# Optimization experiments

Measured on AMD Instinct MI355X. Metric: run time of the kernel, lower is better.

Reference implementation:

```python
import jax, jax.numpy as jnp
import numpy as np

N, L, D, H = 2, 2048, 1024, 16
DK = D // H  # 64


def setup_inputs() -> dict:
    key = jax.random.key(0)
    ks = jax.random.split(key, 8)
    Xq = jax.random.normal(ks[0], (N, L, D), dtype=jnp.float32)
    Xk = jax.random.normal(ks[1], (N, L, D), dtype=jnp.float32)
    Xv = jax.random.normal(ks[2], (N, L, D), dtype=jnp.float32)
    mask_2d = jax.random.randint(ks[3], (N, L, L), 0, 2, dtype=jnp.int32)
    scale = 0.02
    Wq = jax.random.normal(ks[4], (D, D), dtype=jnp.float32) * scale
    Wk = jax.random.normal(ks[5], (D, D), dtype=jnp.float32) * scale
    Wv = jax.random.normal(ks[6], (D, D), dtype=jnp.float32) * scale
    Wo = jax.random.normal(ks[7], (D, D), dtype=jnp.float32) * scale
    return {"Xq": Xq, "Xk": Xk, "Xv": Xv, "Wq": Wq, "Wk": Wk, "Wv": Wv, "Wo": Wo, "mask_2d": mask_2d}


def reference(Xq, Xk, Xv, Wq, Wk, Wv, Wo, mask_2d):
    # Projections (bias=False). Per-head slicing in the original == reshape to [N,L,H,DK].
    Q = (Xq @ Wq).reshape(N, L, H, DK)
    K = (Xk @ Wk).reshape(N, L, H, DK)
    V = (Xv @ Wv).reshape(N, L, H, DK)
    # Scaled dot-product scores: [N, H, L, L]
    scores = jnp.einsum("blhd,bmhd->bhlm", Q, K) / jnp.sqrt(jnp.asarray(DK, scores_dtype(Q)))
    # NOTE: original uses masked_fill(mask==0, 0) BEFORE softmax (zero-fill, not -inf).
    scores = jnp.where(mask_2d[:, None, :, :] == 0, jnp.zeros((), scores.dtype), scores)
    A = jax.nn.softmax(scores, axis=-1)
    O = jnp.einsum("bhlm,bmhd->blhd", A, V).reshape(N, L, D)
    return O @ Wo


def scores_dtype(Q):
    return Q.dtype
```

## Files before the change

kernel.cpp:

```cpp
#include <hip/hip_runtime.h>
#include <hip/hip_bf16.h>

#define NB 2
#define L_SEQ 2048
#define NH 16
#define DKH 64
#define DMODEL 1024
#define MROWS (NB * L_SEQ)
#define QSCALE 0.18033688f
#define DD (DMODEL * DMODEL)

typedef __attribute__((ext_vector_type(8))) short short8;
typedef __attribute__((ext_vector_type(4))) float f32x4;

static __device__ __forceinline__ unsigned short f2bf(float f) {
    unsigned u = __float_as_uint(f);
    u += 0x7fffu + ((u >> 16) & 1u);
    return (unsigned short)(u >> 16);
}

static __device__ __forceinline__ float fexp2(float x) {
#if __has_builtin(__builtin_amdgcn_exp2f)
    return __builtin_amdgcn_exp2f(x);
#else
    return __expf(x * 0.6931471806f);
#endif
}

static __device__ __forceinline__ unsigned pk_bf16(float a, float b) {
    __hip_bfloat162 h = __float22bfloat162_rn(make_float2(a, b));
    return *reinterpret_cast<unsigned*>(&h);
}

static __device__ __forceinline__ void gll16(const void* g, void* l) {
    __builtin_amdgcn_global_load_lds(
        (const __attribute__((address_space(1))) void*)g,
        (__attribute__((address_space(3))) void*)l, 16, 0, 0);
}

__global__ __launch_bounds__(256)
void prep(const float* __restrict__ Xq, const float* __restrict__ Xk,
          const float* __restrict__ Xv, const float* __restrict__ w0,
          const float* __restrict__ w1, const float* __restrict__ w2,
          const float* __restrict__ w3, const int* __restrict__ mask,
          unsigned short* __restrict__ XB, unsigned short* __restrict__ WtB,
          unsigned long long* __restrict__ MWT)
{
    __shared__ float ts[32][33];
    const int bx = blockIdx.x;
    const int t  = threadIdx.x;

    if (bx < 12288) {
        const int z = bx >> 12;
        const float* src = (z == 0) ? Xq : (z == 1) ? Xk : Xv;
        const size_t i4 = (size_t)(bx & 4095) * 256 + t;
        float4 v = ((const float4*)src)[i4];
        ushort4 o;
        o.x = f2bf(v.x); o.y = f2bf(v.y); o.z = f2bf(v.z); o.w = f2bf(v.w);
        ((ushort4*)(XB + (size_t)z * 4194304))[i4] = o;
    } else if (bx < 16384) {
        const int idx = bx - 12288;
        const int z   = idx >> 10;
        const int rem = idx & 1023;
        const float* W = (z == 0) ? w0 : (z == 1) ? w1 : (z == 2) ? w2 : w3;
        unsigned short* Wt = WtB + (size_t)z * DD;
        const int n0 = (rem & 31) * 32;
        const int k0 = (rem >> 5) * 32;
        const int r  = t >> 3;
        const int c  = (t & 7) * 4;
        float4 v = *(const float4*)&W[(size_t)(k0 + r) * DMODEL + n0 + c];
        ts[r][c + 0] = v.x; ts[r][c + 1] = v.y;
        ts[r][c + 2] = v.z; ts[r][c + 3] = v.w;
        __syncthreads();
        ushort4 o;
        o.x = f2bf(ts[c + 0][r]); o.y = f2bf(ts[c + 1][r]);
        o.z = f2bf(ts[c + 2][r]); o.w = f2bf(ts[c + 3][r]);
        *(ushort4*)&Wt[(size_t)(n0 + r) * DMODEL + k0 + c] = o;
    } else {
        const int lane = t & 63;
        const size_t wbase = (size_t)(bx - 16384) * 4 + (t >> 6);
#pragma unroll
        for (int it = 0; it < 8; ++it) {
            const size_t wid = wbase + (size_t)it * 16384;
            const int mv = mask[wid * 64 + lane];
            const unsigned long long bits = __ballot(mv != 0);
            if (lane == 0) {
                const int b   = (int)(wid >> 16);
                const int rem = (int)(wid & 65535);
                const int row = rem >> 5;
                const int wd  = rem & 31;
                MWT[((size_t)b * 32 + wd) * L_SEQ + row] = bits;
            }
        }
    }
}

__global__ __launch_bounds__(256)
void gemm_qkv(const unsigned short* __restrict__ XB,
              const unsigned short* __restrict__ WtB,
              unsigned short* __restrict__ QKV)
{
    __shared__ __align__(16) unsigned short SMEM[16384];

    const int t    = threadIdx.x;
    const int w    = t >> 6;
    const int lane = t & 63;

    const int bid   = blockIdx.x;
    const int xcd   = bid & 7;
    const int idx   = bid >> 3;
    const int pair  = xcd * 12 + (idx >> 3);
    const int n0    = (idx & 7) * 128;
    const int m0    = (pair & 31) * 128;
    const int z     = pair >> 5;

    const unsigned short* A = XB  + (size_t)z * ((size_t)MROWS * DMODEL);
    const unsigned short* B = WtB + (size_t)z * DD;

    const int srow = lane >> 2;
    const int sc4  = (lane & 3) ^ (srow & 3);

    const unsigned short* ag[2];
    const unsigned short* bg[2];
    int lao[2], lbo[2];
#pragma unroll
    for (int g = 0; g < 2; ++g) {
        const int R = w * 32 + g * 16;
        ag[g] = A + (size_t)(m0 + R + srow) * DMODEL + sc4 * 8;
        bg[g] = B + (size_t)(n0 + R + srow) * DMODEL + sc4 * 8;
        lao[g] = R * 32;
        lbo[g] = R * 32;
    }

    const int ml = lane & 15;
    const int q  = lane >> 4;
    const int wm = (w >> 1) * 64;
    const int wn = (w & 1) * 64;

    const f32x4 z4 = {0.f, 0.f, 0.f, 0.f};
    f32x4 acc[4][4];
#pragma unroll
    for (int i = 0; i < 4; ++i)
#pragma unroll
        for (int j = 0; j < 4; ++j) acc[i][j] = z4;

#pragma unroll
    for (int g = 0; g < 2; ++g) {
        gll16(ag[g], &SMEM[lao[g]]);
        gll16(bg[g], &SMEM[8192 + lbo[g]]);
    }

    for (int j = 0; j < 32; ++j) {
        const int cur = j & 1;
        __syncthreads();
        if (j < 31) {
            const int kt = (j + 1) * 32;
            const int nb = (cur ^ 1) * 4096;
#pragma unroll
            for (int g = 0; g < 2; ++g) {
                gll16(ag[g] + kt, &SMEM[nb + lao[g]]);
                gll16(bg[g] + kt, &SMEM[8192 + nb + lbo[g]]);
            }
        }
        const unsigned short* As = &SMEM[cur * 4096];
        const unsigned short* Bs = &SMEM[8192 + cur * 4096];
        short8 av[4], bv[4];
#pragma unroll
        for (int mt = 0; mt < 4; ++mt)
            av[mt] = *(const short8*)
                &As[(wm + mt * 16 + ml) * 32 + ((q ^ (ml & 3)) * 8)];
#pragma unroll
        for (int nt = 0; nt < 4; ++nt)
            bv[nt] = *(const short8*)
                &Bs[(wn + nt * 16 + ml) * 32 + ((q ^ (ml & 3)) * 8)];
#pragma unroll
        for (int mt = 0; mt < 4; ++mt)
#pragma unroll
            for (int nt = 0; nt < 4; ++nt)
                acc[mt][nt] = __builtin_amdgcn_mfma_f32_16x16x32_bf16(
                    av[mt], bv[nt], acc[mt][nt], 0, 0, 0);
    }

    unsigned short* O = QKV + (size_t)z * ((size_t)MROWS * DMODEL);
    __syncthreads();
    unsigned short* Ts = SMEM;

    if (z == 2) {
#pragma unroll
        for (int mt = 0; mt < 4; ++mt) {
            const int trow0 = wm + mt * 16 + q * 4;
            const int ch    = trow0 >> 3;
#pragma unroll
            for (int nt = 0; nt < 4; ++nt) {
                const int tcol = wn + nt * 16 + ml;
                const int pc   = (ch & 8) | ((ch & 7) ^ (tcol & 7));
                ushort4 pv;
                pv.x = f2bf(acc[mt][nt][0]); pv.y = f2bf(acc[mt][nt][1]);
                pv.z = f2bf(acc[mt][nt][2]); pv.w = f2bf(acc[mt][nt][3]);
                *(ushort4*)&Ts[tcol * 128 + pc * 8 + (trow0 & 7)] = pv;
            }
        }
        __syncthreads();
        const int bb = m0 >> 11;
        const int l0 = (m0 & (L_SEQ - 1)) + (t & 15) * 8;
        const int cr = t & 15;
#pragma unroll
        for (int it = 0; it < 8; ++it) {
            const int tcol = (t >> 4) + 16 * it;
            const int pc   = (cr & 8) | ((cr & 7) ^ (tcol & 7));
            short8 vv = *(const short8*)&Ts[tcol * 128 + pc * 8];
            const int n  = n0 + tcol;
            const int hh = n >> 6;
            const int dk = n & (DKH - 1);
            *(short8*)&O[((size_t)(bb * NH + hh) * DKH + dk) * L_SEQ + l0] = vv;
        }
    } else {
        const float qs = (z == 0) ? QSCALE : 1.0f;
#pragma unroll
        for (int mt = 0; mt < 4; ++mt) {
            const int row0 = wm + mt * 16 + q * 4;
#pragma unroll
            for (int nt = 0; nt < 4; ++nt) {
                const int col = wn + nt * 16 + ml;
#pragma unroll
                for (int r = 0; r < 4; ++r)
                    Ts[(row0 + r) * 128 + col] = f2bf(acc[mt][nt][r] * qs);
            }
        }
        __syncthreads();
        const int mloc = t >> 3;
        const int c0   = t & 7;
#pragma unroll
        for (int pass = 0; pass < 4; ++pass) {
#pragma unroll
            for (int half = 0; half < 2; ++half) {
                const int m = mloc + 32 * pass;
                const int c = c0 + 8 * half;
                short8 v = *(const short8*)&Ts[m * 128 + c * 8];
                const int row = m0 + m;
                const int bb  = row >> 11;
                const int l   = row & (L_SEQ - 1);
                const int n   = n0 + c * 8;
                const int hh  = n >> 6;
                const int dk  = n & (DKH - 1);
                *(short8*)&O[(((size_t)(bb * NH + hh) * L_SEQ + l) << 6) + dk] = v;
            }
        }
    }
}

__global__ __launch_bounds__(256)
void gemm_out(const unsigned short* __restrict__ OB,
              const unsigned short* __restrict__ Wt,
              float* __restrict__ out)
{
    __shared__ __align__(16) unsigned short As[2][2048];
    __shared__ __align__(16) unsigned short Bs[2][4096];

    const int t    = threadIdx.x;
    const int w    = t >> 6;
    const int lane = t & 63;

    const int bid = blockIdx.x;
    const int xcd = bid & 7;
    const int idx = bid >> 3;
    const int n0  = (idx & 7) * 128;
    const int m0  = (xcd * 8 + (idx >> 3)) * 64;

    const int srow = lane >> 2;
    const int sc4  = (lane & 3) ^ (srow & 3);

    const unsigned short* ag =
        OB + (size_t)(m0 + w * 16 + srow) * DMODEL + sc4 * 8;
    const unsigned short* bg[2];
    int lbo[2];
#pragma unroll
    for (int g = 0; g < 2; ++g) {
        const int R = w * 32 + g * 16;
        bg[g] = Wt + (size_t)(n0 + R + srow) * DMODEL + sc4 * 8;
        lbo[g] = R * 32;
    }
    const int lao = (w * 16) * 32;

    const int ml = lane & 15;
    const int q  = lane >> 4;
    const int wm = (w >> 1) * 32;
    const int wn = (w & 1) * 64;

    const f32x4 z4 = {0.f, 0.f, 0.f, 0.f};
    f32x4 acc[2][4];
#pragma unroll
    for (int i = 0; i < 2; ++i)
#pragma unroll
        for (int j = 0; j < 4; ++j) acc[i][j] = z4;

    gll16(ag, &As[0][lao]);
#pragma unroll
    for (int g = 0; g < 2; ++g) gll16(bg[g], &Bs[0][lbo[g]]);

    for (int j = 0; j < 32; ++j) {
        const int cur = j & 1;
        __syncthreads();
        if (j < 31) {
            const int kt = (j + 1) * 32;
            gll16(ag + kt, &As[cur ^ 1][lao]);
#pragma unroll
            for (int g = 0; g < 2; ++g)
                gll16(bg[g] + kt, &Bs[cur ^ 1][lbo[g]]);
        }
        short8 av[2], bv[4];
#pragma unroll
        for (int mt = 0; mt < 2; ++mt)
            av[mt] = *(const short8*)
                &As[cur][(wm + mt * 16 + ml) * 32 + ((q ^ (ml & 3)) * 8)];
#pragma unroll
        for (int nt = 0; nt < 4; ++nt)
            bv[nt] = *(const short8*)
                &Bs[cur][(wn + nt * 16 + ml) * 32 + ((q ^ (ml & 3)) * 8)];
#pragma unroll
        for (int mt = 0; mt < 2; ++mt)
#pragma unroll
            for (int nt = 0; nt < 4; ++nt)
                acc[mt][nt] = __builtin_amdgcn_mfma_f32_16x16x32_bf16(
                    av[mt], bv[nt], acc[mt][nt], 0, 0, 0);
    }

#pragma unroll
    for (int mt = 0; mt < 2; ++mt) {
        const int gr0 = m0 + wm + mt * 16 + q * 4;
#pragma unroll
        for (int nt = 0; nt < 4; ++nt) {
            const int col = n0 + wn + nt * 16 + ml;
#pragma unroll
            for (int r = 0; r < 4; ++r)
                out[(size_t)(gr0 + r) * DMODEL + col] = acc[mt][nt][r];
        }
    }
}

__global__ __launch_bounds__(256, 4)
void attn_mfma(const unsigned short* __restrict__ Qb,
               const unsigned short* __restrict__ Kb,
               const unsigned short* __restrict__ Vtb,
               const unsigned long long* __restrict__ MWT,
               unsigned short* __restrict__ OB)
{
    __shared__ __align__(16) unsigned short Qs[64 * 64];
    __shared__ __align__(16) unsigned short Ks[64 * 64];
    __shared__ __align__(16) unsigned short Vts[64 * 64];
    __shared__ __align__(16) unsigned short Ps[4][16 * 64];
    __shared__ __align__(16) unsigned long long MskL[64];

    const int t    = threadIdx.x;
    const int w    = t >> 6;
    const int lane = t & 63;
    const int ml   = lane & 15;
    const int quad = lane >> 4;

    const int bid = blockIdx.x;
    const int p   = (bid >> 8) * 8 + (bid & 7);
    const int jq  = (bid >> 3) & 31;
    const int h   = p & 15;
    const int b   = p >> 4;
    const int q0  = jq * 64;

    const size_t hoff = (size_t)(b * NH + h) * L_SEQ * DKH;
    const unsigned short* Qh  = Qb  + hoff;
    const unsigned short* Kh  = Kb  + hoff;
    const unsigned short* Vth = Vtb + hoff;

    const int srow = lane >> 3;
    const int sc   = (lane & 7) ^ srow;

    gll16(Qh + (size_t)(q0 + w * 16 + srow) * DKH + sc * 8, &Qs[(w * 16) * 64]);
    gll16(Qh + (size_t)(q0 + w * 16 + 8 + srow) * DKH + sc * 8, &Qs[(w * 16 + 8) * 64]);
    __syncthreads();

    short8 qf[2];
#pragma unroll
    for (int s = 0; s < 2; ++s)
        qf[s] = *(const short8*)
            &Qs[(w * 16 + ml) * 64 + (((s * 4 + quad) ^ (ml & 7)) * 8)];

    const unsigned short* kg0 = Kh + (size_t)(w * 16 + srow) * DKH + sc * 8;
    const unsigned short* kg1 = Kh + (size_t)(w * 16 + 8 + srow) * DKH + sc * 8;
    const unsigned short* vg0 = Vth + (size_t)(w * 16 + srow) * L_SEQ + sc * 8;
    const unsigned short* vg1 = Vth + (size_t)(w * 16 + 8 + srow) * L_SEQ + sc * 8;
    unsigned short* lk0 = &Ks[(w * 16) * 64 + lane * 8];
    unsigned short* lk1 = &Ks[(w * 16 + 8) * 64 + lane * 8];
    unsigned short* lv0 = &Vts[(w * 16) * 64 + lane * 8];
    unsigned short* lv1 = &Vts[(w * 16 + 8) * 64 + lane * 8];

    const unsigned long long* mg = MWT + (size_t)b * 32 * L_SEQ + q0 + t;
    unsigned long long m_pf = 0;
    if (t < 64) m_pf = mg[0];

    short8 kr0 = *(const short8*)kg0;  kg0 += 64 * DKH;
    short8 kr1 = *(const short8*)kg1;  kg1 += 64 * DKH;
    short8 vr0 = *(const short8*)vg0;  vg0 += 64;
    short8 vr1 = *(const short8*)vg1;  vg1 += 64;

    f32x4 oacc[4];
    const f32x4 z4 = {0.f, 0.f, 0.f, 0.f};
#pragma unroll
    for (int dt = 0; dt < 4; ++dt) oacc[dt] = z4;
    float l_i = 0.f;

    for (int j = 0; j < 32; ++j) {
        __syncthreads();
        *(short8*)lk0 = kr0;
        *(short8*)lk1 = kr1;
        *(short8*)lv0 = vr0;
        *(short8*)lv1 = vr1;
        if (t < 64) MskL[t] = m_pf;
        __syncthreads();
        if (j < 31) {
            kr0 = *(const short8*)kg0;  kg0 += 64 * DKH;
            kr1 = *(const short8*)kg1;  kg1 += 64 * DKH;
            vr0 = *(const short8*)vg0;  vg0 += 64;
            vr1 = *(const short8*)vg1;  vg1 += 64;
            if (t < 64) m_pf = mg[(size_t)(j + 1) * L_SEQ];
        }

        f32x4 sacc[4];
#pragma unroll
        for (int kt = 0; kt < 4; ++kt) sacc[kt] = z4;
#pragma unroll
        for (int s = 0; s < 2; ++s) {
            short8 kf[4];
#pragma unroll
            for (int kt = 0; kt < 4; ++kt)
                kf[kt] = *(const short8*)
                    &Ks[(kt * 16 + ml) * 64 + (((s * 4 + quad) ^ (ml & 7)) * 8)];
#pragma unroll
            for (int kt = 0; kt < 4; ++kt)
                sacc[kt] = __builtin_amdgcn_mfma_f32_16x16x32_bf16(
                    kf[kt], qf[s], sacc[kt], 0, 0, 0);
        }

        const unsigned long long wq = MskL[w * 16 + ml] >> (quad * 4);
        const unsigned mlo = (unsigned)wq;
        const unsigned mhi = (unsigned)(wq >> 32);
        float rs = 0.f;
        float pr[4][4];
#pragma unroll
        for (int kt = 0; kt < 4; ++kt) {
            const unsigned word = (kt < 2) ? mlo : mhi;
            const int base = (kt & 1) * 16;
#pragma unroll
            for (int r = 0; r < 4; ++r) {
                const float mf = (float)((word >> (base + r)) & 1u);
                const float e  = fexp2(sacc[kt][r] * mf);
                pr[kt][r] = e;
                rs += e;
            }
        }
        rs += __shfl_xor(rs, 16);
        rs += __shfl_xor(rs, 32);
        l_i += rs;
#pragma unroll
        for (int kt = 0; kt < 4; ++kt) {
            uint2 pk;
            pk.x = pk_bf16(pr[kt][0], pr[kt][1]);
            pk.y = pk_bf16(pr[kt][2], pr[kt][3]);
            const int cp = (kt * 2 + (quad >> 1)) ^ (ml & 7);
            *(uint2*)&Ps[w][ml * 64 + cp * 8 + (quad & 1) * 4] = pk;
        }

#pragma unroll
        for (int s = 0; s < 2; ++s) {
            const short8 pf = *(const short8*)
                &Ps[w][ml * 64 + (((s * 4 + quad) ^ (ml & 7)) * 8)];
#pragma unroll
            for (int dt = 0; dt < 4; ++dt) {
                const short8 vf = *(const short8*)
                    &Vts[(dt * 16 + ml) * 64 + (((s * 4 + quad) ^ (ml & 7)) * 8)];
                oacc[dt] = __builtin_amdgcn_mfma_f32_16x16x32_bf16(
                    vf, pf, oacc[dt], 0, 0, 0);
            }
        }
    }

    const float inv = 1.0f / l_i;
    const int qrow = q0 + w * 16 + ml;
#pragma unroll
    for (int dt = 0; dt < 4; ++dt) {
        ushort4 o4;
        o4.x = f2bf(oacc[dt][0] * inv);
        o4.y = f2bf(oacc[dt][1] * inv);
        o4.z = f2bf(oacc[dt][2] * inv);
        o4.w = f2bf(oacc[dt][3] * inv);
        *(ushort4*)&OB[(size_t)(b * L_SEQ + qrow) * DMODEL + h * DKH +
                       dt * 16 + quad * 4] = o4;
    }
}

extern "C" void kernel_launch(void* const* d_in, const int* in_sizes, int n_in,
                              void* d_out, int out_size, void* d_ws, size_t ws_size,
                              hipStream_t stream)
{
    (void)in_sizes; (void)n_in; (void)out_size; (void)ws_size;

    const float* Xq   = (const float*)d_in[0];
    const float* Xk   = (const float*)d_in[1];
    const float* Xv   = (const float*)d_in[2];
    const float* Wq   = (const float*)d_in[3];
    const float* Wk   = (const float*)d_in[4];
    const float* Wv   = (const float*)d_in[5];
    const float* Wo   = (const float*)d_in[6];
    const int*   mask = (const int*)d_in[7];
    float* out = (float*)d_out;

    char* base = (char*)d_ws;
    unsigned short*     XB  = (unsigned short*)base;
    unsigned short*     WtB = (unsigned short*)(base + (24u << 20));
    unsigned short*     QKV = (unsigned short*)(base + (32u << 20));
    unsigned short*     OB  = (unsigned short*)(base + (56u << 20));
    unsigned long long* MWT = (unsigned long long*)(base + (64u << 20));

    const size_t tsz = (size_t)MROWS * DMODEL;

    prep<<<dim3(20480), 256, 0, stream>>>(
        Xq, Xk, Xv, Wq, Wk, Wv, Wo, mask, XB, WtB, MWT);

    gemm_qkv<<<dim3(768), 256, 0, stream>>>(XB, WtB, QKV);

    attn_mfma<<<dim3(1024), 256, 0, stream>>>(
        QKV, QKV + tsz, QKV + 2 * tsz, MWT, OB);

    gemm_out<<<dim3(512), 256, 0, stream>>>(OB, WtB + 3 * (size_t)DD, out);
}
```

Baseline: 256.6 us.

## Process 128 queries per attention block with double-buffered K/V tiles

Each attention block now handles 128 query rows (32 per wave) instead of 64, so every K/V tile staged in LDS feeds twice as many MFMAs and K/V global traffic is halved. K, V and mask tiles are double-buffered in LDS, which leaves one barrier per iteration instead of two. Block-to-head mapping is redone so heads are grouped per XCD, and Q is staged through the K buffer. The costs are more registers (launch bounds drop to 2 blocks per CU), half as many blocks in the grid, and fewer waves available to hide latency.

Result: no change. 261.2 us (+1.8%).

```diff
diff --git a/kernel.cpp b/kernel.cpp
--- a/kernel.cpp
+++ b/kernel.cpp
@@ -338,18 +338,17 @@
     }
 }
 
-__global__ __launch_bounds__(256, 4)
+__global__ __launch_bounds__(256, 2)
 void attn_mfma(const unsigned short* __restrict__ Qb,
                const unsigned short* __restrict__ Kb,
                const unsigned short* __restrict__ Vtb,
                const unsigned long long* __restrict__ MWT,
                unsigned short* __restrict__ OB)
 {
-    __shared__ __align__(16) unsigned short Qs[64 * 64];
-    __shared__ __align__(16) unsigned short Ks[64 * 64];
-    __shared__ __align__(16) unsigned short Vts[64 * 64];
-    __shared__ __align__(16) unsigned short Ps[4][16 * 64];
-    __shared__ __align__(16) unsigned long long MskL[64];
+    __shared__ __align__(16) unsigned short Ks[2][64 * 64];
+    __shared__ __align__(16) unsigned short Vts[2][64 * 64];
+    __shared__ __align__(16) unsigned short Ps[4][32 * 64];
+    __shared__ __align__(16) unsigned long long MskL[2][128];
 
     const int t    = threadIdx.x;
     const int w    = t >> 6;
@@ -358,11 +357,13 @@
     const int quad = lane >> 4;
 
     const int bid = blockIdx.x;
-    const int p   = (bid >> 8) * 8 + (bid & 7);
-    const int jq  = (bid >> 3) & 31;
+    const int xcd = bid & 7;
+    const int idx = bid >> 3;
+    const int p   = xcd * 4 + (idx >> 4);
+    const int jq  = idx & 15;
     const int h   = p & 15;
     const int b   = p >> 4;
-    const int q0  = jq * 64;
+    const int q0  = jq * 128;
 
     const size_t hoff = (size_t)(b * NH + h) * L_SEQ * DKH;
     const unsigned short* Qh  = Qb  + hoff;
@@ -372,126 +373,170 @@
     const int srow = lane >> 3;
     const int sc   = (lane & 7) ^ srow;
 
-    gll16(Qh + (size_t)(q0 + w * 16 + srow) * DKH + sc * 8, &Qs[(w * 16) * 64]);
-    gll16(Qh + (size_t)(q0 + w * 16 + 8 + srow) * DKH + sc * 8, &Qs[(w * 16 + 8) * 64]);
-    __syncthreads();
-
-    short8 qf[2];
-#pragma unroll
-    for (int s = 0; s < 2; ++s)
-        qf[s] = *(const short8*)
-            &Qs[(w * 16 + ml) * 64 + (((s * 4 + quad) ^ (ml & 7)) * 8)];
+    unsigned short* QL = &Ks[0][0];
+#pragma unroll
+    for (int g = 0; g < 4; ++g)
+        gll16(Qh + (size_t)(q0 + w * 32 + g * 8 + srow) * DKH + sc * 8,
+              &QL[(w * 32 + g * 8) * 64]);
 
     const unsigned short* kg0 = Kh + (size_t)(w * 16 + srow) * DKH + sc * 8;
     const unsigned short* kg1 = Kh + (size_t)(w * 16 + 8 + srow) * DKH + sc * 8;
     const unsigned short* vg0 = Vth + (size_t)(w * 16 + srow) * L_SEQ + sc * 8;
     const unsigned short* vg1 = Vth + (size_t)(w * 16 + 8 + srow) * L_SEQ + sc * 8;
-    unsigned short* lk0 = &Ks[(w * 16) * 64 + lane * 8];
-    unsigned short* lk1 = &Ks[(w * 16 + 8) * 64 + lane * 8];
-    unsigned short* lv0 = &Vts[(w * 16) * 64 + lane * 8];
-    unsigned short* lv1 = &Vts[(w * 16 + 8) * 64 + lane * 8];
-
-    const unsigned long long* mg = MWT + (size_t)b * 32 * L_SEQ + q0 + t;
-    unsigned long long m_pf = 0;
-    if (t < 64) m_pf = mg[0];
 
     short8 kr0 = *(const short8*)kg0;  kg0 += 64 * DKH;
     short8 kr1 = *(const short8*)kg1;  kg1 += 64 * DKH;
     short8 vr0 = *(const short8*)vg0;  vg0 += 64;
     short8 vr1 = *(const short8*)vg1;  vg1 += 64;
 
-    f32x4 oacc[4];
+    const unsigned long long* mg = MWT + (size_t)b * 32 * L_SEQ + q0 + t;
+    unsigned long long m_pf = 0;
+    if (t < 128) m_pf = mg[0];
+
+    __syncthreads();
+
+    short8 qf[2][2];
+#pragma unroll
+    for (int qn = 0; qn < 2; ++qn)
+#pragma unroll
+        for (int s = 0; s < 2; ++s)
+            qf[qn][s] = *(const short8*)
+                &QL[(w * 32 + qn * 16 + ml) * 64 +
+                    (((s * 4 + quad) ^ (ml & 7)) * 8)];
+
+    __syncthreads();
+
+    *(short8*)&Ks[0][(w * 16) * 64 + lane * 8]      = kr0;
+    *(short8*)&Ks[0][(w * 16 + 8) * 64 + lane * 8]  = kr1;
+    *(short8*)&Vts[0][(w * 16) * 64 + lane * 8]     = vr0;
+    *(short8*)&Vts[0][(w * 16 + 8) * 64 + lane * 8] = vr1;
+    if (t < 128) MskL[0][t] = m_pf;
+
+    kr0 = *(const short8*)kg0;  kg0 += 64 * DKH;
+    kr1 = *(const short8*)kg1;  kg1 += 64 * DKH;
+    vr0 = *(const short8*)vg0;  vg0 += 64;
+    vr1 = *(const short8*)vg1;  vg1 += 64;
+    if (t < 128) m_pf = mg[L_SEQ];
+
+    f32x4 oacc[2][4];
     const f32x4 z4 = {0.f, 0.f, 0.f, 0.f};
 #pragma unroll
-    for (int dt = 0; dt < 4; ++dt) oacc[dt] = z4;
-    float l_i = 0.f;
+    for (int qn = 0; qn < 2; ++qn)
+#pragma unroll
+        for (int dt = 0; dt < 4; ++dt) oacc[qn][dt] = z4;
+    float l_i[2] = {0.f, 0.f};
+
+    __syncthreads();
 
     for (int j = 0; j < 32; ++j) {
-        __syncthreads();
-        *(short8*)lk0 = kr0;
-        *(short8*)lk1 = kr1;
-        *(short8*)lv0 = vr0;
-        *(short8*)lv1 = vr1;
-        if (t < 64) MskL[t] = m_pf;
-        __syncthreads();
+        const int cur = j & 1;
         if (j < 31) {
-            kr0 = *(const short8*)kg0;  kg0 += 64 * DKH;
-            kr1 = *(const short8*)kg1;  kg1 += 64 * DKH;
-            vr0 = *(const short8*)vg0;  vg0 += 64;
-            vr1 = *(const short8*)vg1;  vg1 += 64;
-            if (t < 64) m_pf = mg[(size_t)(j + 1) * L_SEQ];
-        }
-
-        f32x4 sacc[4];
-#pragma unroll
-        for (int kt = 0; kt < 4; ++kt) sacc[kt] = z4;
+            const int nxt = cur ^ 1;
+            *(short8*)&Ks[nxt][(w * 16) * 64 + lane * 8]      = kr0;
+            *(short8*)&Ks[nxt][(w * 16 + 8) * 64 + lane * 8]  = kr1;
+            *(short8*)&Vts[nxt][(w * 16) * 64 + lane * 8]     = vr0;
+            *(short8*)&Vts[nxt][(w * 16 + 8) * 64 + lane * 8] = vr1;
+            if (t < 128) MskL[nxt][t] = m_pf;
+            if (j < 30) {
+                kr0 = *(const short8*)kg0;  kg0 += 64 * DKH;
+                kr1 = *(const short8*)kg1;  kg1 += 64 * DKH;
+                vr0 = *(const short8*)vg0;  vg0 += 64;
+                vr1 = *(const short8*)vg1;  vg1 += 64;
+                if (t < 128) m_pf = mg[(size_t)(j + 2) * L_SEQ];
+            }
+        }
+
+        f32x4 sacc[2][4];
+#pragma unroll
+        for (int qn = 0; qn < 2; ++qn)
+#pragma unroll
+            for (int kt = 0; kt < 4; ++kt) sacc[qn][kt] = z4;
 #pragma unroll
         for (int s = 0; s < 2; ++s) {
             short8 kf[4];
 #pragma unroll
             for (int kt = 0; kt < 4; ++kt)
                 kf[kt] = *(const short8*)
-                    &Ks[(kt * 16 + ml) * 64 + (((s * 4 + quad) ^ (ml & 7)) * 8)];
-#pragma unroll
-            for (int kt = 0; kt < 4; ++kt)
-                sacc[kt] = __builtin_amdgcn_mfma_f32_16x16x32_bf16(
-                    kf[kt], qf[s], sacc[kt], 0, 0, 0);
-        }
-
-        const unsigned long long wq = MskL[w * 16 + ml] >> (quad * 4);
-        const unsigned mlo = (unsigned)wq;
-        const unsigned mhi = (unsigned)(wq >> 32);
-        float rs = 0.f;
-        float pr[4][4];
-#pragma unroll
-        for (int kt = 0; kt < 4; ++kt) {
-            const unsigned word = (kt < 2) ? mlo : mhi;
-            const int base = (kt & 1) * 16;
-#pragma unroll
-            for (int r = 0; r < 4; ++r) {
-                const float mf = (float)((word >> (base + r)) & 1u);
-                const float e  = fexp2(sacc[kt][r] * mf);
-                pr[kt][r] = e;
-                rs += e;
-            }
-        }
-        rs += __shfl_xor(rs, 16);
-        rs += __shfl_xor(rs, 32);
-        l_i += rs;
-#pragma unroll
-        for (int kt = 0; kt < 4; ++kt) {
-            uint2 pk;
-            pk.x = pk_bf16(pr[kt][0], pr[kt][1]);
-            pk.y = pk_bf16(pr[kt][2], pr[kt][3]);
-            const int cp = (kt * 2 + (quad >> 1)) ^ (ml & 7);
-            *(uint2*)&Ps[w][ml * 64 + cp * 8 + (quad & 1) * 4] = pk;
+                    &Ks[cur][(kt * 16 + ml) * 64 +
+                             (((s * 4 + quad) ^ (ml & 7)) * 8)];
+#pragma unroll
+            for (int qn = 0; qn < 2; ++qn)
+#pragma unroll
+                for (int kt = 0; kt < 4; ++kt)
+                    sacc[qn][kt] = __builtin_amdgcn_mfma_f32_16x16x32_bf16(
+                        kf[kt], qf[qn][s], sacc[qn][kt], 0, 0, 0);
+        }
+
+#pragma unroll
+        for (int qn = 0; qn < 2; ++qn) {
+            const unsigned long long wq =
+                MskL[cur][w * 32 + qn * 16 + ml] >> (quad * 4);
+            const unsigned mlo = (unsigned)wq;
+            const unsigned mhi = (unsigned)(wq >> 32);
+            float rs = 0.f;
+            float pr[4][4];
+#pragma unroll
+            for (int kt = 0; kt < 4; ++kt) {
+                const unsigned word = (kt < 2) ? mlo : mhi;
+                const int base = (kt & 1) * 16;
+#pragma unroll
+                for (int r = 0; r < 4; ++r) {
+                    const float mf = (float)((word >> (base + r)) & 1u);
+                    const float e  = fexp2(sacc[qn][kt][r] * mf);
+                    pr[kt][r] = e;
+                    rs += e;
+                }
+            }
+            rs += __shfl_xor(rs, 16);
+            rs += __shfl_xor(rs, 32);
+            l_i[qn] += rs;
+#pragma unroll
+            for (int kt = 0; kt < 4; ++kt) {
+                uint2 pk;
+                pk.x = pk_bf16(pr[kt][0], pr[kt][1]);
+                pk.y = pk_bf16(pr[kt][2], pr[kt][3]);
+                const int cp = (kt * 2 + (quad >> 1)) ^ (ml & 7);
+                *(uint2*)&Ps[w][(qn * 16 + ml) * 64 + cp * 8 + (quad & 1) * 4] = pk;
+            }
         }
 
 #pragma unroll
         for (int s = 0; s < 2; ++s) {
-            const short8 pf = *(const short8*)
-                &Ps[w][ml * 64 + (((s * 4 + quad) ^ (ml & 7)) * 8)];
-#pragma unroll
-            for (int dt = 0; dt < 4; ++dt) {
-                const short8 vf = *(const short8*)
-                    &Vts[(dt * 16 + ml) * 64 + (((s * 4 + quad) ^ (ml & 7)) * 8)];
-                oacc[dt] = __builtin_amdgcn_mfma_f32_16x16x32_bf16(
-                    vf, pf, oacc[dt], 0, 0, 0);
-            }
-        }
-    }
-
-    const float inv = 1.0f / l_i;
-    const int qrow = q0 + w * 16 + ml;
-#pragma unroll
-    for (int dt = 0; dt < 4; ++dt) {
-        ushort4 o4;
-        o4.x = f2bf(oacc[dt][0] * inv);
-        o4.y = f2bf(oacc[dt][1] * inv);
-        o4.z = f2bf(oacc[dt][2] * inv);
-        o4.w = f2bf(oacc[dt][3] * inv);
-        *(ushort4*)&OB[(size_t)(b * L_SEQ + qrow) * DMODEL + h * DKH +
-                       dt * 16 + quad * 4] = o4;
+            short8 vf[4];
+#pragma unroll
+            for (int dt = 0; dt < 4; ++dt)
+                vf[dt] = *(const short8*)
+                    &Vts[cur][(dt * 16 + ml) * 64 +
+                              (((s * 4 + quad) ^ (ml & 7)) * 8)];
+#pragma unroll
+            for (int qn = 0; qn < 2; ++qn) {
+                const short8 pf = *(const short8*)
+                    &Ps[w][(qn * 16 + ml) * 64 +
+                           (((s * 4 + quad) ^ (ml & 7)) * 8)];
+#pragma unroll
+                for (int dt = 0; dt < 4; ++dt)
+                    oacc[qn][dt] = __builtin_amdgcn_mfma_f32_16x16x32_bf16(
+                        vf[dt], pf, oacc[qn][dt], 0, 0, 0);
+            }
+        }
+
+        __syncthreads();
+    }
+
+#pragma unroll
+    for (int qn = 0; qn < 2; ++qn) {
+        const float inv = 1.0f / l_i[qn];
+        const int qrow = q0 + w * 32 + qn * 16 + ml;
+#pragma unroll
+        for (int dt = 0; dt < 4; ++dt) {
+            ushort4 o4;
+            o4.x = f2bf(oacc[qn][dt][0] * inv);
+            o4.y = f2bf(oacc[qn][dt][1] * inv);
+            o4.z = f2bf(oacc[qn][dt][2] * inv);
+            o4.w = f2bf(oacc[qn][dt][3] * inv);
+            *(ushort4*)&OB[(size_t)(b * L_SEQ + qrow) * DMODEL + h * DKH +
+                           dt * 16 + quad * 4] = o4;
+        }
     }
 }
 
@@ -525,7 +570,7 @@
 
     gemm_qkv<<<dim3(768), 256, 0, stream>>>(XB, WtB, QKV);
 
-    attn_mfma<<<dim3(1024), 256, 0, stream>>>(
+    attn_mfma<<<dim3(512), 256, 0, stream>>>(
         QKV, QKV + tsz, QKV + 2 * tsz, MWT, OB);
 
     gemm_out<<<dim3(512), 256, 0, stream>>>(OB, WtB + 3 * (size_t)DD, out);
```

## Double-buffer K/V tiles in attention and use 128-query blocks of 512 threads

Applied to the files above, without the earlier changes.

The attention kernel now processes 128 query rows per block with 8 waves, so each loaded K/V tile is shared by twice as many queries. K, V and mask tiles are double-buffered in LDS, which cuts the two barriers per iteration down to one and lets the store of the next tile overlap compute on the current one. The Q staging buffer reuses the K buffer, and the block-to-head mapping is changed so each XCD gets contiguous heads. In exchange, LDS use per block rises and the grid is halved, which may lower occupancy.

New measurement: 247.8 us. 1.04x faster.

```diff
diff --git a/kernel.cpp b/kernel.cpp
--- a/kernel.cpp
+++ b/kernel.cpp
@@ -338,18 +338,17 @@
     }
 }
 
-__global__ __launch_bounds__(256, 4)
+__global__ __launch_bounds__(512, 4)
 void attn_mfma(const unsigned short* __restrict__ Qb,
                const unsigned short* __restrict__ Kb,
                const unsigned short* __restrict__ Vtb,
                const unsigned long long* __restrict__ MWT,
                unsigned short* __restrict__ OB)
 {
-    __shared__ __align__(16) unsigned short Qs[64 * 64];
-    __shared__ __align__(16) unsigned short Ks[64 * 64];
-    __shared__ __align__(16) unsigned short Vts[64 * 64];
-    __shared__ __align__(16) unsigned short Ps[4][16 * 64];
-    __shared__ __align__(16) unsigned long long MskL[64];
+    __shared__ __align__(16) unsigned short Ks[2][64 * 64];
+    __shared__ __align__(16) unsigned short Vts[2][64 * 64];
+    __shared__ __align__(16) unsigned short Ps[8][16 * 64];
+    __shared__ __align__(16) unsigned long long MskL[2][128];
 
     const int t    = threadIdx.x;
     const int w    = t >> 6;
@@ -358,11 +357,13 @@
     const int quad = lane >> 4;
 
     const int bid = blockIdx.x;
-    const int p   = (bid >> 8) * 8 + (bid & 7);
-    const int jq  = (bid >> 3) & 31;
+    const int xcd = bid & 7;
+    const int idx = bid >> 3;
+    const int p   = xcd * 4 + (idx >> 4);
+    const int jq  = idx & 15;
     const int h   = p & 15;
     const int b   = p >> 4;
-    const int q0  = jq * 64;
+    const int q0  = jq * 128;
 
     const size_t hoff = (size_t)(b * NH + h) * L_SEQ * DKH;
     const unsigned short* Qh  = Qb  + hoff;
@@ -372,33 +373,39 @@
     const int srow = lane >> 3;
     const int sc   = (lane & 7) ^ srow;
 
-    gll16(Qh + (size_t)(q0 + w * 16 + srow) * DKH + sc * 8, &Qs[(w * 16) * 64]);
-    gll16(Qh + (size_t)(q0 + w * 16 + 8 + srow) * DKH + sc * 8, &Qs[(w * 16 + 8) * 64]);
+    unsigned short* QL = &Ks[0][0];
+    gll16(Qh + (size_t)(q0 + w * 16 + srow) * DKH + sc * 8,
+          &QL[(w * 16) * 64]);
+    gll16(Qh + (size_t)(q0 + w * 16 + 8 + srow) * DKH + sc * 8,
+          &QL[(w * 16 + 8) * 64]);
+
+    const unsigned short* kg = Kh + (size_t)(w * 8 + srow) * DKH + sc * 8;
+    const unsigned short* vg = Vth + (size_t)(w * 8 + srow) * L_SEQ + sc * 8;
+
+    short8 kr = *(const short8*)kg;  kg += 64 * DKH;
+    short8 vr = *(const short8*)vg;  vg += 64;
+
+    const unsigned long long* mg = MWT + (size_t)b * 32 * L_SEQ + q0 + t;
+    unsigned long long m_pf = 0;
+    if (t < 128) m_pf = mg[0];
+
     __syncthreads();
 
     short8 qf[2];
 #pragma unroll
     for (int s = 0; s < 2; ++s)
         qf[s] = *(const short8*)
-            &Qs[(w * 16 + ml) * 64 + (((s * 4 + quad) ^ (ml & 7)) * 8)];
-
-    const unsigned short* kg0 = Kh + (size_t)(w * 16 + srow) * DKH + sc * 8;
-    const unsigned short* kg1 = Kh + (size_t)(w * 16 + 8 + srow) * DKH + sc * 8;
-    const unsigned short* vg0 = Vth + (size_t)(w * 16 + srow) * L_SEQ + sc * 8;
-    const unsigned short* vg1 = Vth + (size_t)(w * 16 + 8 + srow) * L_SEQ + sc * 8;
-    unsigned short* lk0 = &Ks[(w * 16) * 64 + lane * 8];
-    unsigned short* lk1 = &Ks[(w * 16 + 8) * 64 + lane * 8];
-    unsigned short* lv0 = &Vts[(w * 16) * 64 + lane * 8];
-    unsigned short* lv1 = &Vts[(w * 16 + 8) * 64 + lane * 8];
-
-    const unsigned long long* mg = MWT + (size_t)b * 32 * L_SEQ + q0 + t;
-    unsigned long long m_pf = 0;
-    if (t < 64) m_pf = mg[0];
-
-    short8 kr0 = *(const short8*)kg0;  kg0 += 64 * DKH;
-    short8 kr1 = *(const short8*)kg1;  kg1 += 64 * DKH;
-    short8 vr0 = *(const short8*)vg0;  vg0 += 64;
-    short8 vr1 = *(const short8*)vg1;  vg1 += 64;
+            &QL[(w * 16 + ml) * 64 + (((s * 4 + quad) ^ (ml & 7)) * 8)];
+
+    __syncthreads();
+
+    *(short8*)&Ks[0][(w * 8) * 64 + lane * 8]  = kr;
+    *(short8*)&Vts[0][(w * 8) * 64 + lane * 8] = vr;
+    if (t < 128) MskL[0][t] = m_pf;
+
+    kr = *(const short8*)kg;  kg += 64 * DKH;
+    vr = *(const short8*)vg;  vg += 64;
+    if (t < 128) m_pf = mg[L_SEQ];
 
     f32x4 oacc[4];
     const f32x4 z4 = {0.f, 0.f, 0.f, 0.f};
@@ -406,20 +413,20 @@
     for (int dt = 0; dt < 4; ++dt) oacc[dt] = z4;
     float l_i = 0.f;
 
+    __syncthreads();
+
     for (int j = 0; j < 32; ++j) {
-        __syncthreads();
-        *(short8*)lk0 = kr0;
-        *(short8*)lk1 = kr1;
-        *(short8*)lv0 = vr0;
-        *(short8*)lv1 = vr1;
-        if (t < 64) MskL[t] = m_pf;
-        __syncthreads();
+        const int cur = j & 1;
         if (j < 31) {
-            kr0 = *(const short8*)kg0;  kg0 += 64 * DKH;
-            kr1 = *(const short8*)kg1;  kg1 += 64 * DKH;
-            vr0 = *(const short8*)vg0;  vg0 += 64;
-            vr1 = *(const short8*)vg1;  vg1 += 64;
-            if (t < 64) m_pf = mg[(size_t)(j + 1) * L_SEQ];
+            const int nxt = cur ^ 1;
+            *(short8*)&Ks[nxt][(w * 8) * 64 + lane * 8]  = kr;
+            *(short8*)&Vts[nxt][(w * 8) * 64 + lane * 8] = vr;
+            if (t < 128) MskL[nxt][t] = m_pf;
+            if (j < 30) {
+                kr = *(const short8*)kg;  kg += 64 * DKH;
+                vr = *(const short8*)vg;  vg += 64;
+                if (t < 128) m_pf = mg[(size_t)(j + 2) * L_SEQ];
+            }
         }
 
         f32x4 sacc[4];
@@ -431,14 +438,15 @@
 #pragma unroll
             for (int kt = 0; kt < 4; ++kt)
                 kf[kt] = *(const short8*)
-                    &Ks[(kt * 16 + ml) * 64 + (((s * 4 + quad) ^ (ml & 7)) * 8)];
+                    &Ks[cur][(kt * 16 + ml) * 64 +
+                             (((s * 4 + quad) ^ (ml & 7)) * 8)];
 #pragma unroll
             for (int kt = 0; kt < 4; ++kt)
                 sacc[kt] = __builtin_amdgcn_mfma_f32_16x16x32_bf16(
                     kf[kt], qf[s], sacc[kt], 0, 0, 0);
         }
 
-        const unsigned long long wq = MskL[w * 16 + ml] >> (quad * 4);
+        const unsigned long long wq = MskL[cur][w * 16 + ml] >> (quad * 4);
         const unsigned mlo = (unsigned)wq;
         const unsigned mhi = (unsigned)(wq >> 32);
         float rs = 0.f;
@@ -474,11 +482,14 @@
 #pragma unroll
             for (int dt = 0; dt < 4; ++dt) {
                 const short8 vf = *(const short8*)
-                    &Vts[(dt * 16 + ml) * 64 + (((s * 4 + quad) ^ (ml & 7)) * 8)];
+                    &Vts[cur][(dt * 16 + ml) * 64 +
+                              (((s * 4 + quad) ^ (ml & 7)) * 8)];
                 oacc[dt] = __builtin_amdgcn_mfma_f32_16x16x32_bf16(
                     vf, pf, oacc[dt], 0, 0, 0);
             }
         }
+
+        __syncthreads();
     }
 
     const float inv = 1.0f / l_i;
@@ -525,7 +536,7 @@
 
     gemm_qkv<<<dim3(768), 256, 0, stream>>>(XB, WtB, QKV);
 
-    attn_mfma<<<dim3(1024), 256, 0, stream>>>(
+    attn_mfma<<<dim3(512), 512, 0, stream>>>(
         QKV, QKV + tsz, QKV + 2 * tsz, MWT, OB);
 
     gemm_out<<<dim3(512), 256, 0, stream>>>(OB, WtB + 3 * (size_t)DD, out);
```
